# Kernel tuning notes

Hardware: AMD Instinct MI355X
Metric: run time of the kernel (lower is better)

The kernel has to match this reference:

```python
import jax, jax.numpy as jnp
import numpy as np


def setup_inputs() -> dict:
    key = jax.random.key(0)
    ks = jax.random.split(key, 16)
    B, S, D = 2, 2048, 1024
    H, SH, RH = 16, 1, 3
    hd = D // H
    w = 1.0 / np.sqrt(D)
    return {
        "x": jax.random.normal(ks[0], (B, S, D), jnp.float32),
        "Wq": jax.random.normal(ks[1], (D, D), jnp.float32) * w,
        "bq": jnp.zeros((D,), jnp.float32),
        "Wk": jax.random.normal(ks[2], (D, D), jnp.float32) * w,
        "bk": jnp.zeros((D,), jnp.float32),
        "Wv": jax.random.normal(ks[3], (D, D), jnp.float32) * w,
        "bv": jnp.zeros((D,), jnp.float32),
        "Wproj": jax.random.normal(ks[4], (D, D), jnp.float32) * w,
        "bproj": jnp.zeros((D,), jnp.float32),
        "Wr": jax.random.normal(ks[5], (D, H - SH), jnp.float32) * w,
        "br": jnp.zeros((H - SH,), jnp.float32),
        "Ws": jax.random.normal(ks[6], (D, 2), jnp.float32) * w,
        "bs": jnp.zeros((2,), jnp.float32),
        "temperature": jnp.zeros((H, 1, 1), jnp.float32),
        "query_embedding": jax.random.truncated_normal(ks[7], -2.0, 2.0, (H, 1, hd), jnp.float32) * 0.02,
        "num_heads": H,
        "shared_heads": SH,
        "routed_heads": RH,
    }


def reference(x, Wq, bq, Wk, bk, Wv, bv, Wproj, bproj, Wr, br, Ws, bs,
              temperature, query_embedding, num_heads, shared_heads, routed_heads):
    B, S, D = x.shape
    H = num_heads
    hd = D // H

    def split_heads(t):  # [B,S,D] -> [B,H,S,hd]
        return t.reshape(B, S, H, hd).transpose(0, 2, 1, 3)

    q = split_heads(x @ Wq + bq)
    k = split_heads(x @ Wk + bk)
    v = split_heads(x @ Wv + bv)

    # L2-normalize q along head_dim, add learned query embedding, scale by softplus(temperature)
    q_norm = q * jax.lax.rsqrt(jnp.sum(q * q, axis=-1, keepdims=True) + 1e-12)
    q_scaled = (q_norm + query_embedding[None]) * jax.nn.softplus(temperature)[None]

    attn = jnp.einsum('bhqd,bhkd->bhqk', q_scaled, k) / jnp.sqrt(jnp.float32(hd))
    attn = jax.nn.softmax(attn, axis=-1)
    o = jnp.einsum('bhqk,bhkd->bhqd', attn, v)
    o = o.transpose(0, 2, 1, 3).reshape(B, S, D)  # [B,S,D]

    # Routed-head gating via top-k router
    gates = jax.nn.softmax(o @ Wr + br, axis=-1)          # [B,S,H-SH]
    _, idx = jax.lax.top_k(gates, routed_heads)           # [B,S,RH]
    mask = jax.nn.one_hot(idx, H - shared_heads, dtype=gates.dtype).sum(axis=2)
    routed_gates = gates * mask * jnp.float32(routed_heads)

    # Shared-head gating
    sw = jax.nn.softmax(o @ Ws + bs, axis=-1)             # [B,S,2]
    shared_gates = sw * jnp.float32(shared_heads)
    w0 = sw * 2.0
    shared_gates = w0[..., 0:1] * shared_gates
    routed_gates = w0[..., 1:2] * routed_gates
    masked_gates = jnp.concatenate([shared_gates, routed_gates], axis=-1)

    # einsum('bnh,bnd->bnd') sums over h: scales o by sum of gates
    o = masked_gates.sum(axis=-1, keepdims=True) * o
    return o @ Wproj + bproj
```

## Files before the change

kernel.cpp:

```cpp
#include <hip/hip_runtime.h>
#include <hip/hip_bf16.h>

typedef unsigned short ushort_t;
typedef unsigned int uint_t;

typedef __attribute__((ext_vector_type(8))) short bf8;
typedef __attribute__((ext_vector_type(4))) float f4;
typedef __attribute__((ext_vector_type(16))) float f16v;

__device__ __forceinline__ float bf2f(ushort_t u) {
    unsigned int x = ((unsigned int)u) << 16;
    return __uint_as_float(x);
}
__device__ __forceinline__ ushort_t f2bf(float f) {
    unsigned int x = __float_as_uint(f);
    unsigned int r = x + 0x7fffu + ((x >> 16) & 1u);
    return (ushort_t)(r >> 16);
}
__device__ __forceinline__ uint_t pack2bf(float a, float b) {
    return (uint_t)f2bf(a) | ((uint_t)f2bf(b) << 16);
}
__device__ __forceinline__ uint_t pack2bf_fast(float a, float b) {
    uint_t au = __float_as_uint(a) + 0x8000u;
    uint_t bu = __float_as_uint(b) + 0x8000u;
    return __builtin_amdgcn_perm(bu, au, 0x07060302);
}
__device__ __forceinline__ float exp2_fast(float x) {
    float r; asm("v_exp_f32 %0, %1" : "=v"(r) : "v"(x)); return r;
}
__device__ __forceinline__ uint_t cvtpk_bf16(float lo, float hi) {
    uint_t r; asm("v_cvt_pk_bf16_f32 %0, %1, %2" : "=v"(r) : "v"(lo), "v"(hi)); return r;
}
__device__ __forceinline__ void pl32swap(uint_t &a, uint_t &b) {
    asm("v_permlane32_swap_b32 %0, %1" : "+v"(a), "+v"(b));
}

__device__ __forceinline__ void gl2lds16(const ushort_t* g, ushort_t* l) {
    __builtin_amdgcn_global_load_lds(
        (const __attribute__((address_space(1))) void*)g,
        (__attribute__((address_space(3))) void*)l, 16, 0, 0);
}

__global__ __launch_bounds__(256)
void prep(const float* __restrict__ x, ushort_t* __restrict__ xb,
          const float* __restrict__ Wr, const float* __restrict__ Ws,
          ushort_t* __restrict__ Wg,
          const float* __restrict__ W0, const float* __restrict__ W1,
          const float* __restrict__ W2, const float* __restrict__ W3,
          ushort_t* __restrict__ T0, ushort_t* __restrict__ T1,
          ushort_t* __restrict__ T2, ushort_t* __restrict__ T3)
{
    __shared__ float tile[32][33];
    int bid = blockIdx.x;
    int t = threadIdx.x;
    if (bid < 4096) {
        int i = bid * 256 + t;
        float4 v = ((const float4*)x)[i];
        uint2 o;
        o.x = pack2bf(v.x, v.y);
        o.y = pack2bf(v.z, v.w);
        ((uint2*)xb)[i] = o;
    } else if (bid < 4224) {
        int idx = (bid - 4096) * 256 + t;
        int c = idx >> 10, d = idx & 1023;
        float v = 0.f;
        if (c < 15) v = Wr[(size_t)d * 15 + c];
        else if (c < 17) v = Ws[(size_t)d * 2 + (c - 15)];
        Wg[idx] = f2bf(v);
    } else {
        int idx = bid - 4224;
        int z = idx >> 10, r10 = idx & 1023;
        int k0 = (r10 & 31) * 32, n0 = (r10 >> 5) * 32;
        const float* W; ushort_t* T;
        switch (z) {
            case 0: W = W0; T = T0; break;
            case 1: W = W1; T = T1; break;
            case 2: W = W2; T = T2; break;
            default: W = W3; T = T3; break;
        }
        int r = t >> 3, c4 = (t & 7) * 4;
        float4 v = *(const float4*)&W[(size_t)(k0 + r) * 1024 + n0 + c4];
        tile[r][c4 + 0] = v.x; tile[r][c4 + 1] = v.y;
        tile[r][c4 + 2] = v.z; tile[r][c4 + 3] = v.w;
        __syncthreads();
        int n = t >> 3, kk = (t & 7) * 4;
        uint2 o;
        o.x = pack2bf(tile[kk][n], tile[kk + 1][n]);
        o.y = pack2bf(tile[kk + 2][n], tile[kk + 3][n]);
        *(uint2*)&T[(size_t)(n0 + n) * 1024 + k0 + kk] = o;
    }
}

__global__ __launch_bounds__(256)
void gemmQKV(const ushort_t* __restrict__ A, const ushort_t* __restrict__ Wt3,
             const float* __restrict__ bq, const float* __restrict__ bk,
             const float* __restrict__ bv,
             ushort_t* __restrict__ Qb, ushort_t* __restrict__ Kw,
             ushort_t* __restrict__ VTw,
             const float* __restrict__ temp, const float* __restrict__ emb)
{
    const int K = 1024;
    __shared__ ushort_t As[128 * 64];
    __shared__ ushort_t Bs[128 * 64];

    int t = threadIdx.x;
    int m0 = blockIdx.x * 128;
    int y = blockIdx.y;
    int region = y >> 3;
    int n0 = (y & 7) * 128;

    int lane = t & 63, w = t >> 6;
    int lm = lane & 15, quad = lane >> 4;
    int wm = (w >> 1) * 64, wn = (w & 1) * 64;

    f4 acc[4][4] = {};

    int srow = t >> 3;
    int schunk = ((t & 7) ^ (srow & 7)) * 8;
    const ushort_t* pA = &A[(size_t)(m0 + srow) * K + schunk];
    const ushort_t* pB = &Wt3[(size_t)(y * 128 + srow) * K + schunk];
    const size_t rstep = (size_t)32 * K;

    for (int k0 = 0; k0 < K; k0 += 64) {
        #pragma unroll
        for (int j = 0; j < 4; j++) {
            gl2lds16(pA + j * rstep, &As[(t + j * 256) * 8]);
            gl2lds16(pB + j * rstep, &Bs[(t + j * 256) * 8]);
        }
        pA += 64; pB += 64;
        __syncthreads();

        #pragma unroll
        for (int ks = 0; ks < 2; ks++) {
            int rc = ((ks * 4 + quad) ^ (lm & 7)) * 8;
            bf8 af[4], bfr[4];
            #pragma unroll
            for (int mi = 0; mi < 4; mi++)
                af[mi] = *(bf8*)&As[(wm + mi * 16 + lm) * 64 + rc];
            #pragma unroll
            for (int ni = 0; ni < 4; ni++)
                bfr[ni] = *(bf8*)&Bs[(wn + ni * 16 + lm) * 64 + rc];
            if (region == 2) {
                #pragma unroll
                for (int mi = 0; mi < 4; mi++)
                #pragma unroll
                for (int ni = 0; ni < 4; ni++)
                    acc[mi][ni] = __builtin_amdgcn_mfma_f32_16x16x32_bf16(af[mi], bfr[ni], acc[mi][ni], 0, 0, 0);
            } else {
                #pragma unroll
                for (int ni = 0; ni < 4; ni++)
                #pragma unroll
                for (int mi = 0; mi < 4; mi++)
                    acc[ni][mi] = __builtin_amdgcn_mfma_f32_16x16x32_bf16(bfr[ni], af[mi], acc[ni][mi], 0, 0, 0);
            }
        }
        __syncthreads();
    }

    if (region == 0) {
        int head = (n0 + wn) >> 6;
        float sp = log1pf(__expf(temp[head]));
        float qs = sp * 0.18033688011112042f;
        f4 bv4[4], ev4[4];
        #pragma unroll
        for (int ni = 0; ni < 4; ni++) {
            bv4[ni] = *(const f4*)&bq[n0 + wn + ni * 16 + quad * 4];
            ev4[ni] = *(const f4*)&emb[head * 64 + ni * 16 + quad * 4];
        }
        #pragma unroll
        for (int mi = 0; mi < 4; mi++) {
            float v[4][4];
            float ss = 0.f;
            #pragma unroll
            for (int ni = 0; ni < 4; ni++)
            #pragma unroll
            for (int i = 0; i < 4; i++) {
                v[ni][i] = acc[ni][mi][i] + bv4[ni][i];
                ss += v[ni][i] * v[ni][i];
            }
            ss += __shfl_xor(ss, 16, 64);
            ss += __shfl_xor(ss, 32, 64);
            float rs = rsqrtf(ss + 1e-12f);
            int tok = m0 + wm + mi * 16 + lm;
            int b = tok >> 11, s = tok & 2047;
            size_t rowb = (((size_t)(b * 16 + head)) * 2048 + s) * 64;
            #pragma unroll
            for (int ni = 0; ni < 4; ni++) {
                uint2 o;
                o.x = pack2bf((v[ni][0] * rs + ev4[ni][0]) * qs,
                              (v[ni][1] * rs + ev4[ni][1]) * qs);
                o.y = pack2bf((v[ni][2] * rs + ev4[ni][2]) * qs,
                              (v[ni][3] * rs + ev4[ni][3]) * qs);
                *(uint2*)&Qb[rowb + ni * 16 + quad * 4] = o;
            }
        }
    } else if (region == 1) {
        int head = (n0 + wn) >> 6;
        f4 bv4[4];
        #pragma unroll
        for (int ni = 0; ni < 4; ni++)
            bv4[ni] = *(const f4*)&bk[n0 + wn + ni * 16 + quad * 4];
        #pragma unroll
        for (int mi = 0; mi < 4; mi++) {
            int tok = m0 + wm + mi * 16 + lm;
            int b = tok >> 11, s = tok & 2047;
            size_t rowb = (((size_t)(b * 16 + head)) * 2048 + s) * 64;
            #pragma unroll
            for (int ni = 0; ni < 4; ni++) {
                uint2 o;
                o.x = pack2bf(acc[ni][mi][0] + bv4[ni][0], acc[ni][mi][1] + bv4[ni][1]);
                o.y = pack2bf(acc[ni][mi][2] + bv4[ni][2], acc[ni][mi][3] + bv4[ni][3]);
                *(uint2*)&Kw[rowb + ni * 16 + quad * 4] = o;
            }
        }
    } else {
        float bvv[4];
        #pragma unroll
        for (int ni = 0; ni < 4; ni++) bvv[ni] = bv[n0 + wn + ni * 16 + lm];
        #pragma unroll
        for (int mi = 0; mi < 4; mi++) {
            int gr0 = m0 + wm + mi * 16 + quad * 4;
            int b = gr0 >> 11, s0 = gr0 & 2047;
            #pragma unroll
            for (int ni = 0; ni < 4; ni++) {
                int gc = n0 + wn + ni * 16 + lm;
                int h = gc >> 6, d = gc & 63;
                uint2 o;
                o.x = pack2bf(acc[mi][ni][0] + bvv[ni], acc[mi][ni][1] + bvv[ni]);
                o.y = pack2bf(acc[mi][ni][2] + bvv[ni], acc[mi][ni][3] + bvv[ni]);
                *(uint2*)&VTw[(((size_t)(b * 16 + h)) * 64 + d) * 2048 + s0] = o;
            }
        }
    }
}

__global__ __launch_bounds__(256)
void gemmP(const ushort_t* __restrict__ A, const ushort_t* __restrict__ Wt,
           const float* __restrict__ bias, const float* __restrict__ G,
           float* __restrict__ out, int M, int N, int K)
{
    __shared__ ushort_t As[128 * 64];
    __shared__ ushort_t Bs[128 * 64];

    int t = threadIdx.x;
    int m0 = blockIdx.x * 128, n0 = blockIdx.y * 128;
    int lane = t & 63, w = t >> 6;
    int lm = lane & 15, quad = lane >> 4;
    int wm = (w >> 1) * 64, wn = (w & 1) * 64;

    f4 acc[4][4] = {};

    int srow = t >> 3;
    int schunk = ((t & 7) ^ (srow & 7)) * 8;
    const ushort_t* pA = &A[(size_t)(m0 + srow) * K + schunk];
    const ushort_t* pB = &Wt[(size_t)(n0 + srow) * K + schunk];
    const size_t rstep = (size_t)32 * K;

    for (int k0 = 0; k0 < K; k0 += 64) {
        #pragma unroll
        for (int j = 0; j < 4; j++) {
            gl2lds16(pA + j * rstep, &As[(t + j * 256) * 8]);
            gl2lds16(pB + j * rstep, &Bs[(t + j * 256) * 8]);
        }
        pA += 64; pB += 64;
        __syncthreads();

        #pragma unroll
        for (int ks = 0; ks < 2; ks++) {
            int rc = ((ks * 4 + quad) ^ (lm & 7)) * 8;
            bf8 af[4], bfr[4];
            #pragma unroll
            for (int mi = 0; mi < 4; mi++)
                af[mi] = *(bf8*)&As[(wm + mi * 16 + lm) * 64 + rc];
            #pragma unroll
            for (int ni = 0; ni < 4; ni++)
                bfr[ni] = *(bf8*)&Bs[(wn + ni * 16 + lm) * 64 + rc];
            #pragma unroll
            for (int ni = 0; ni < 4; ni++)
            #pragma unroll
            for (int mi = 0; mi < 4; mi++)
                acc[ni][mi] = __builtin_amdgcn_mfma_f32_16x16x32_bf16(bfr[ni], af[mi], acc[ni][mi], 0, 0, 0);
        }
        __syncthreads();
    }

    f4 bv4[4];
    #pragma unroll
    for (int ni = 0; ni < 4; ni++)
        bv4[ni] = *(const f4*)&bias[n0 + wn + ni * 16 + quad * 4];
    #pragma unroll
    for (int mi = 0; mi < 4; mi++) {
        int tok = m0 + wm + mi * 16 + lm;
        float g = G[tok];
        size_t rowb = (size_t)tok * N + n0 + wn;
        #pragma unroll
        for (int ni = 0; ni < 4; ni++) {
            f4 o;
            #pragma unroll
            for (int i = 0; i < 4; i++) o[i] = g * acc[ni][mi][i] + bv4[ni][i];
            *(f4*)&out[rowb + ni * 16 + quad * 4] = o;
        }
    }
}

__global__ __launch_bounds__(256)
void attn(const ushort_t* __restrict__ Q, const ushort_t* __restrict__ K,
          const ushort_t* __restrict__ VT, ushort_t* __restrict__ Opart,
          float* __restrict__ Lw)
{
    __shared__ ushort_t Ks[64 * 72];
    __shared__ ushort_t Vt[64 * 72];

    int t = threadIdx.x, lane = t & 63, w = t >> 6;
    int l31 = lane & 31;
    uint_t hi = lane >> 5;
    int bid = blockIdx.x;
    int bh = bid & 31, qt = (bid >> 5) & 15, ks = bid >> 9;
    size_t base = (size_t)bh * 2048 * 64;

    int tok = qt * 128 + w * 32 + l31;
    const ushort_t* qp = &Q[base + (size_t)tok * 64 + hi * 8];
    bf8 qa[4];
    #pragma unroll
    for (int c = 0; c < 4; c++) qa[c] = *(const bf8*)(qp + c * 16);

    float l_part = 0.f;
    f16v o_acc[2] = {};

    int sr = t >> 3, sc = (t & 7) * 8;
    const ushort_t* kp = &K[base + (size_t)(ks * 1024 + sr) * 64 + sc];
    const ushort_t* vp = &VT[base + (size_t)sr * 2048 + ks * 1024 + sc];

    uint4 rk0 = *(const uint4*)(kp);
    uint4 rk1 = *(const uint4*)(kp + 32 * 64);
    uint4 rv0 = *(const uint4*)(vp);
    uint4 rv1 = *(const uint4*)(vp + 32 * 2048);
    kp += 64 * 64; vp += 64;

    for (int it = 0; it < 16; ++it) {
        *(uint4*)&Ks[sr * 72 + sc] = rk0;
        *(uint4*)&Ks[(sr + 32) * 72 + sc] = rk1;
        *(uint4*)&Vt[sr * 72 + sc] = rv0;
        *(uint4*)&Vt[(sr + 32) * 72 + sc] = rv1;
        __syncthreads();

        rk0 = *(const uint4*)(kp);
        rk1 = *(const uint4*)(kp + 32 * 64);
        rv0 = *(const uint4*)(vp);
        rv1 = *(const uint4*)(vp + 32 * 2048);
        kp += 64 * 64; vp += 64;

        bf8 pf[4];
        #pragma unroll
        for (int kt2 = 0; kt2 < 2; kt2++) {
            f16v s = {};
            #pragma unroll
            for (int c = 0; c < 4; c++) {
                bf8 kf = *(bf8*)&Ks[(kt2 * 32 + l31) * 72 + c * 16 + hi * 8];
                s = __builtin_amdgcn_mfma_f32_32x32x16_bf16(kf, qa[c], s, 0, 0, 0);
            }
            uint_t px[4], py[4];
            #pragma unroll
            for (int g = 0; g < 4; g++) {
                float p0 = exp2_fast(s[g * 4 + 0]);
                float p1 = exp2_fast(s[g * 4 + 1]);
                float p2 = exp2_fast(s[g * 4 + 2]);
                float p3 = exp2_fast(s[g * 4 + 3]);
                l_part += (p0 + p1) + (p2 + p3);
                px[g] = cvtpk_bf16(p0, p1);
                py[g] = cvtpk_bf16(p2, p3);
            }
            #pragma unroll
            for (int cc = 0; cc < 2; cc++) {
                uint_t ax = px[2 * cc], bx = px[2 * cc + 1];
                uint_t ay = py[2 * cc], by = py[2 * cc + 1];
                pl32swap(ax, bx);
                pl32swap(ay, by);
                uint4 u;
                u.x = ax; u.y = ay; u.z = bx; u.w = by;
                pf[kt2 * 2 + cc] = *(bf8*)&u;
            }
        }

        #pragma unroll
        for (int c = 0; c < 4; c++) {
            #pragma unroll
            for (int dt = 0; dt < 2; dt++) {
                bf8 vf = *(bf8*)&Vt[(dt * 32 + l31) * 72 + c * 16 + hi * 8];
                o_acc[dt] = __builtin_amdgcn_mfma_f32_32x32x16_bf16(vf, pf[c], o_acc[dt], 0, 0, 0);
            }
        }
        __syncthreads();
    }

    l_part += __shfl_xor(l_part, 32, 64);
    if (hi == 0) Lw[((size_t)ks * 32 + bh) * 2048 + tok] = l_part;

    size_t pbase = (((size_t)(ks * 32 + bh)) * 2048 + tok) * 64;
    #pragma unroll
    for (int dt = 0; dt < 2; dt++)
    #pragma unroll
    for (int g = 0; g < 4; g++) {
        int d0 = dt * 32 + g * 8 + hi * 4;
        uint2 o;
        o.x = pack2bf_fast(o_acc[dt][g * 4 + 0], o_acc[dt][g * 4 + 1]);
        o.y = pack2bf_fast(o_acc[dt][g * 4 + 2], o_acc[dt][g * 4 + 3]);
        *(uint2*)&Opart[pbase + d0] = o;
    }
}

__global__ __launch_bounds__(256)
void combine(const ushort_t* __restrict__ Opart, const float* __restrict__ Lw,
             ushort_t* __restrict__ Ob)
{
    int i = blockIdx.x * 256 + threadIdx.x;
    int flat = i * 4;
    int row = flat >> 6;
    int d = flat & 63;
    int bh = row >> 11, tok = row & 2047;
    int b = bh >> 4, h = bh & 15;
    float rl = 1.f / (Lw[row] + Lw[65536 + row]);
    uint2 p0 = *(const uint2*)&Opart[flat];
    uint2 p1 = *(const uint2*)&Opart[4194304 + flat];
    float v0 = (bf2f(p0.x & 0xffff) + bf2f(p1.x & 0xffff)) * rl;
    float v1 = (bf2f(p0.x >> 16)   + bf2f(p1.x >> 16))   * rl;
    float v2 = (bf2f(p0.y & 0xffff) + bf2f(p1.y & 0xffff)) * rl;
    float v3 = (bf2f(p0.y >> 16)   + bf2f(p1.y >> 16))   * rl;
    uint2 o;
    o.x = pack2bf(v0, v1);
    o.y = pack2bf(v2, v3);
    *(uint2*)&Ob[((size_t)(b * 2048 + tok)) * 1024 + h * 64 + d] = o;
}

__global__ __launch_bounds__(256)
void router(const ushort_t* __restrict__ O, const ushort_t* __restrict__ Wg,
            const float* __restrict__ br, const float* __restrict__ bs,
            float* __restrict__ G)
{
    __shared__ float Ls[64][21];
    int t = threadIdx.x, lane = t & 63, w = t >> 6;
    int lm = lane & 15, quad = lane >> 4;
    int tok0 = blockIdx.x * 64;

    const ushort_t* ap = &O[(size_t)(tok0 + w * 16 + lm) * 1024 + quad * 8];
    const ushort_t* b0p = &Wg[(size_t)lm * 1024 + quad * 8];
    const ushort_t* b1p = &Wg[(size_t)(16 + lm) * 1024 + quad * 8];

    f4 acc0 = {}, acc1 = {};
    for (int k0 = 0; k0 < 1024; k0 += 32) {
        bf8 a = *(const bf8*)(ap + k0);
        bf8 b0 = *(const bf8*)(b0p + k0);
        bf8 b1 = *(const bf8*)(b1p + k0);
        acc0 = __builtin_amdgcn_mfma_f32_16x16x32_bf16(a, b0, acc0, 0, 0, 0);
        acc1 = __builtin_amdgcn_mfma_f32_16x16x32_bf16(a, b1, acc1, 0, 0, 0);
    }
    #pragma unroll
    for (int i = 0; i < 4; i++) {
        int tl = w * 16 + quad * 4 + i;
        Ls[tl][lm] = acc0[i];
        if (lm == 0) Ls[tl][16] = acc1[i];
    }
    __syncthreads();
    if (t < 64) {
        float v[15];
        float mx = -1e30f;
        #pragma unroll
        for (int c = 0; c < 15; c++) { v[c] = Ls[t][c] + br[c]; mx = fmaxf(mx, v[c]); }
        float sum = 0.f;
        #pragma unroll
        for (int c = 0; c < 15; c++) { v[c] = __expf(v[c] - mx); sum += v[c]; }
        float inv = 1.f / sum;
        float t3 = 0.f;
        for (int r = 0; r < 3; r++) {
            int bi = 0; float bv = -1e30f;
            #pragma unroll
            for (int c = 0; c < 15; c++) if (v[c] > bv) { bv = v[c]; bi = c; }
            t3 += bv; v[bi] = -1e30f;
        }
        t3 *= inv;
        float a0 = Ls[t][15] + bs[0], a1 = Ls[t][16] + bs[1];
        float m2 = fmaxf(a0, a1);
        float e0 = __expf(a0 - m2), e1 = __expf(a1 - m2);
        G[tok0 + t] = (2.f * e0 + 6.f * e1 * t3) / (e0 + e1);
    }
}

extern "C" void kernel_launch(void* const* d_in, const int* in_sizes, int n_in,
                              void* d_out, int out_size, void* d_ws, size_t ws_size,
                              hipStream_t stream)
{
    const float* x     = (const float*)d_in[0];
    const float* Wq    = (const float*)d_in[1];
    const float* bq    = (const float*)d_in[2];
    const float* Wk    = (const float*)d_in[3];
    const float* bk    = (const float*)d_in[4];
    const float* Wv    = (const float*)d_in[5];
    const float* bv    = (const float*)d_in[6];
    const float* Wproj = (const float*)d_in[7];
    const float* bproj = (const float*)d_in[8];
    const float* Wr    = (const float*)d_in[9];
    const float* br    = (const float*)d_in[10];
    const float* Ws    = (const float*)d_in[11];
    const float* bs    = (const float*)d_in[12];
    const float* temp  = (const float*)d_in[13];
    const float* emb   = (const float*)d_in[14];

    const int M = 4096, N = 1024, Kd = 1024;

    char* ws = (char*)d_ws;
    ushort_t* Kw    = (ushort_t*)ws;
    ushort_t* VTw   = (ushort_t*)(ws + 8388608);
    ushort_t* Qb    = (ushort_t*)(ws + 16777216);
    ushort_t* Wtp   = (ushort_t*)(ws + 25165824);
    float*    Gw    = (float*)(ws + 27262976);
    ushort_t* Wg    = (ushort_t*)(ws + 27279360);
    float*    Lw    = (float*)(ws + 27344896);
    ushort_t* Wt3   = (ushort_t*)(ws + 27869184);
    ushort_t* xb    = (ushort_t*)(ws + 34160640);
    ushort_t* Opart = (ushort_t*)(ws + 27869184);
    ushort_t* Ob    = Qb;

    prep<<<8320, 256, 0, stream>>>(x, xb, Wr, Ws, Wg, Wq, Wk, Wv, Wproj,
        Wt3, Wt3 + 1048576, Wt3 + 2097152, Wtp);

    gemmQKV<<<dim3(32, 24), 256, 0, stream>>>(xb, Wt3, bq, bk, bv,
        Qb, Kw, VTw, temp, emb);

    attn<<<1024, 256, 0, stream>>>(Qb, Kw, VTw, Opart, Lw);

    combine<<<4096, 256, 0, stream>>>(Opart, Lw, Ob);

    router<<<64, 256, 0, stream>>>(Ob, Wg, br, bs, Gw);

    gemmP<<<dim3(32, 8), 256, 0, stream>>>(Ob, Wtp, bproj, Gw, (float*)d_out, M, N, Kd);
}
```

Measured before the change: 245.2 us.

## Double-buffer LDS tiles with async prefetch in QKV and projection GEMMs

Both GEMM kernels move from single-buffered LDS tiles, which loaded and synchronized every K step, to two LDS buffers. Each iteration loads all fragments for the tile into registers, issues the global-to-LDS loads for tile kt+2 into the freed buffer, then runs the MFMAs at raised priority. Explicit vmcnt/lgkmcnt waits and barriers replace __syncthreads, so global loads overlap with compute. LDS use doubles to 64KB per block, which may reduce occupancy, and fragment registers double.

```diff
diff --git a/kernel.cpp b/kernel.cpp
--- a/kernel.cpp
+++ b/kernel.cpp
@@ -39,6 +39,19 @@
     __builtin_amdgcn_global_load_lds(
         (const __attribute__((address_space(1))) void*)g,
         (__attribute__((address_space(3))) void*)l, 16, 0, 0);
+}
+
+__device__ __forceinline__ void waitv8() {
+    asm volatile("s_waitcnt vmcnt(8)" ::: "memory");
+    __builtin_amdgcn_sched_barrier(0);
+}
+__device__ __forceinline__ void waitv0() {
+    asm volatile("s_waitcnt vmcnt(0)" ::: "memory");
+    __builtin_amdgcn_sched_barrier(0);
+}
+__device__ __forceinline__ void waitl0() {
+    asm volatile("s_waitcnt lgkmcnt(0)" ::: "memory");
+    __builtin_amdgcn_sched_barrier(0);
 }
 
 __global__ __launch_bounds__(256)
@@ -100,8 +113,9 @@
              const float* __restrict__ temp, const float* __restrict__ emb)
 {
     const int K = 1024;
-    __shared__ ushort_t As[128 * 64];
-    __shared__ ushort_t Bs[128 * 64];
+    const int NT = 16;
+    __shared__ ushort_t As[2][128 * 64];
+    __shared__ ushort_t Bs[2][128 * 64];
 
     int t = threadIdx.x;
     int m0 = blockIdx.x * 128;
@@ -117,44 +131,76 @@
 
     int srow = t >> 3;
     int schunk = ((t & 7) ^ (srow & 7)) * 8;
-    const ushort_t* pA = &A[(size_t)(m0 + srow) * K + schunk];
-    const ushort_t* pB = &Wt3[(size_t)(y * 128 + srow) * K + schunk];
+    const ushort_t* pA0 = &A[(size_t)(m0 + srow) * K + schunk];
+    const ushort_t* pB0 = &Wt3[(size_t)(y * 128 + srow) * K + schunk];
     const size_t rstep = (size_t)32 * K;
 
-    for (int k0 = 0; k0 < K; k0 += 64) {
-        #pragma unroll
-        for (int j = 0; j < 4; j++) {
-            gl2lds16(pA + j * rstep, &As[(t + j * 256) * 8]);
-            gl2lds16(pB + j * rstep, &Bs[(t + j * 256) * 8]);
-        }
-        pA += 64; pB += 64;
-        __syncthreads();
-
+    #pragma unroll
+    for (int j = 0; j < 4; j++) {
+        gl2lds16(pA0 + j * rstep, &As[0][(t + j * 256) * 8]);
+        gl2lds16(pB0 + j * rstep, &Bs[0][(t + j * 256) * 8]);
+    }
+    __builtin_amdgcn_sched_barrier(0);
+    #pragma unroll
+    for (int j = 0; j < 4; j++) {
+        gl2lds16(pA0 + 64 + j * rstep, &As[1][(t + j * 256) * 8]);
+        gl2lds16(pB0 + 64 + j * rstep, &Bs[1][(t + j * 256) * 8]);
+    }
+    __builtin_amdgcn_sched_barrier(0);
+    waitv8();
+    __builtin_amdgcn_s_barrier();
+
+    int cur = 0;
+    for (int kt = 0; kt < NT; ++kt) {
+        bf8 af[2][4], bfr[2][4];
         #pragma unroll
         for (int ks = 0; ks < 2; ks++) {
             int rc = ((ks * 4 + quad) ^ (lm & 7)) * 8;
-            bf8 af[4], bfr[4];
             #pragma unroll
             for (int mi = 0; mi < 4; mi++)
-                af[mi] = *(bf8*)&As[(wm + mi * 16 + lm) * 64 + rc];
+                af[ks][mi] = *(bf8*)&As[cur][(wm + mi * 16 + lm) * 64 + rc];
             #pragma unroll
             for (int ni = 0; ni < 4; ni++)
-                bfr[ni] = *(bf8*)&Bs[(wn + ni * 16 + lm) * 64 + rc];
+                bfr[ks][ni] = *(bf8*)&Bs[cur][(wn + ni * 16 + lm) * 64 + rc];
+        }
+        waitl0();
+        __builtin_amdgcn_s_barrier();
+
+        if (kt + 2 < NT) {
+            const ushort_t* sA = pA0 + (kt + 2) * 64;
+            const ushort_t* sB = pB0 + (kt + 2) * 64;
+            #pragma unroll
+            for (int j = 0; j < 4; j++) {
+                gl2lds16(sA + j * rstep, &As[cur][(t + j * 256) * 8]);
+                gl2lds16(sB + j * rstep, &Bs[cur][(t + j * 256) * 8]);
+            }
+        }
+        __builtin_amdgcn_sched_barrier(0);
+
+        __builtin_amdgcn_s_setprio(1);
+        #pragma unroll
+        for (int ks = 0; ks < 2; ks++) {
             if (region == 2) {
                 #pragma unroll
                 for (int mi = 0; mi < 4; mi++)
                 #pragma unroll
                 for (int ni = 0; ni < 4; ni++)
-                    acc[mi][ni] = __builtin_amdgcn_mfma_f32_16x16x32_bf16(af[mi], bfr[ni], acc[mi][ni], 0, 0, 0);
+                    acc[mi][ni] = __builtin_amdgcn_mfma_f32_16x16x32_bf16(af[ks][mi], bfr[ks][ni], acc[mi][ni], 0, 0, 0);
             } else {
                 #pragma unroll
                 for (int ni = 0; ni < 4; ni++)
                 #pragma unroll
                 for (int mi = 0; mi < 4; mi++)
-                    acc[ni][mi] = __builtin_amdgcn_mfma_f32_16x16x32_bf16(bfr[ni], af[mi], acc[ni][mi], 0, 0, 0);
-            }
-        }
-        __syncthreads();
+                    acc[ni][mi] = __builtin_amdgcn_mfma_f32_16x16x32_bf16(bfr[ks][ni], af[ks][mi], acc[ni][mi], 0, 0, 0);
+            }
+        }
+        __builtin_amdgcn_s_setprio(0);
+        __builtin_amdgcn_sched_barrier(0);
+
+        if (kt + 2 < NT) waitv8();
+        else             waitv0();
+        __builtin_amdgcn_s_barrier();
+        cur ^= 1;
     }
 
     if (region == 0) {
@@ -239,8 +285,9 @@
            const float* __restrict__ bias, const float* __restrict__ G,
            float* __restrict__ out, int M, int N, int K)
 {
-    __shared__ ushort_t As[128 * 64];
-    __shared__ ushort_t Bs[128 * 64];
+    const int NT = 16;
+    __shared__ ushort_t As[2][128 * 64];
+    __shared__ ushort_t Bs[2][128 * 64];
 
     int t = threadIdx.x;
     int m0 = blockIdx.x * 128, n0 = blockIdx.y * 128;
@@ -252,36 +299,68 @@
 
     int srow = t >> 3;
     int schunk = ((t & 7) ^ (srow & 7)) * 8;
-    const ushort_t* pA = &A[(size_t)(m0 + srow) * K + schunk];
-    const ushort_t* pB = &Wt[(size_t)(n0 + srow) * K + schunk];
+    const ushort_t* pA0 = &A[(size_t)(m0 + srow) * K + schunk];
+    const ushort_t* pB0 = &Wt[(size_t)(n0 + srow) * K + schunk];
     const size_t rstep = (size_t)32 * K;
 
-    for (int k0 = 0; k0 < K; k0 += 64) {
-        #pragma unroll
-        for (int j = 0; j < 4; j++) {
-            gl2lds16(pA + j * rstep, &As[(t + j * 256) * 8]);
-            gl2lds16(pB + j * rstep, &Bs[(t + j * 256) * 8]);
-        }
-        pA += 64; pB += 64;
-        __syncthreads();
-
+    #pragma unroll
+    for (int j = 0; j < 4; j++) {
+        gl2lds16(pA0 + j * rstep, &As[0][(t + j * 256) * 8]);
+        gl2lds16(pB0 + j * rstep, &Bs[0][(t + j * 256) * 8]);
+    }
+    __builtin_amdgcn_sched_barrier(0);
+    #pragma unroll
+    for (int j = 0; j < 4; j++) {
+        gl2lds16(pA0 + 64 + j * rstep, &As[1][(t + j * 256) * 8]);
+        gl2lds16(pB0 + 64 + j * rstep, &Bs[1][(t + j * 256) * 8]);
+    }
+    __builtin_amdgcn_sched_barrier(0);
+    waitv8();
+    __builtin_amdgcn_s_barrier();
+
+    int cur = 0;
+    for (int kt = 0; kt < NT; ++kt) {
+        bf8 af[2][4], bfr[2][4];
         #pragma unroll
         for (int ks = 0; ks < 2; ks++) {
             int rc = ((ks * 4 + quad) ^ (lm & 7)) * 8;
-            bf8 af[4], bfr[4];
             #pragma unroll
             for (int mi = 0; mi < 4; mi++)
-                af[mi] = *(bf8*)&As[(wm + mi * 16 + lm) * 64 + rc];
+                af[ks][mi] = *(bf8*)&As[cur][(wm + mi * 16 + lm) * 64 + rc];
             #pragma unroll
             for (int ni = 0; ni < 4; ni++)
-                bfr[ni] = *(bf8*)&Bs[(wn + ni * 16 + lm) * 64 + rc];
+                bfr[ks][ni] = *(bf8*)&Bs[cur][(wn + ni * 16 + lm) * 64 + rc];
+        }
+        waitl0();
+        __builtin_amdgcn_s_barrier();
+
+        if (kt + 2 < NT) {
+            const ushort_t* sA = pA0 + (kt + 2) * 64;
+            const ushort_t* sB = pB0 + (kt + 2) * 64;
+            #pragma unroll
+            for (int j = 0; j < 4; j++) {
+                gl2lds16(sA + j * rstep, &As[cur][(t + j * 256) * 8]);
+                gl2lds16(sB + j * rstep, &Bs[cur][(t + j * 256) * 8]);
+            }
+        }
+        __builtin_amdgcn_sched_barrier(0);
+
+        __builtin_amdgcn_s_setprio(1);
+        #pragma unroll
+        for (int ks = 0; ks < 2; ks++) {
             #pragma unroll
             for (int ni = 0; ni < 4; ni++)
             #pragma unroll
             for (int mi = 0; mi < 4; mi++)
-                acc[ni][mi] = __builtin_amdgcn_mfma_f32_16x16x32_bf16(bfr[ni], af[mi], acc[ni][mi], 0, 0, 0);
-        }
-        __syncthreads();
+                acc[ni][mi] = __builtin_amdgcn_mfma_f32_16x16x32_bf16(bfr[ks][ni], af[ks][mi], acc[ni][mi], 0, 0, 0);
+        }
+        __builtin_amdgcn_s_setprio(0);
+        __builtin_amdgcn_sched_barrier(0);
+
+        if (kt + 2 < NT) waitv8();
+        else             waitv0();
+        __builtin_amdgcn_s_barrier();
+        cur ^= 1;
     }
 
     f4 bv4[4];
```

New measurement: 248.3 us. About the same (+1.3%).

## Fuse split-K combine with router and remap GEMM blocks for XCD locality

Applied to the files above, without the earlier changes.

Merges the combine and router kernels into one kernel. Each block merges the split-K attention partials for 16 tokens, keeps the bf16 rows in LDS, and runs the router MFMA and gating softmax/top-k from there, so Ob is not re-read from global memory. It also flattens the GEMM grids and remaps block indices so that blocks on the same XCD (index mod 8) work on nearby M/N tiles, aiming for better L2 reuse. The trade-off is that the fused kernel launches only 256 blocks and one wave does the serial router GEMM while the other three wait, so it may run below full occupancy.

```diff
diff --git a/kernel.cpp b/kernel.cpp
--- a/kernel.cpp
+++ b/kernel.cpp
@@ -39,6 +39,11 @@
     __builtin_amdgcn_global_load_lds(
         (const __attribute__((address_space(1))) void*)g,
         (__attribute__((address_space(3))) void*)l, 16, 0, 0);
+}
+
+__device__ __forceinline__ void waitl0() {
+    asm volatile("s_waitcnt lgkmcnt(0)" ::: "memory");
+    __builtin_amdgcn_sched_barrier(0);
 }
 
 __global__ __launch_bounds__(256)
@@ -104,8 +109,13 @@
     __shared__ ushort_t Bs[128 * 64];
 
     int t = threadIdx.x;
-    int m0 = blockIdx.x * 128;
-    int y = blockIdx.y;
+    int n = blockIdx.x;
+    int c = n & 7, m = n >> 3;
+    int cx = c & 3, cy = c >> 2;
+    int xi = m & 7, yi = m >> 3;
+    int bx = cx * 8 + xi;
+    int y  = cy * 12 + yi;
+    int m0 = bx * 128;
     int region = y >> 3;
     int n0 = (y & 7) * 128;
 
@@ -243,7 +253,12 @@
     __shared__ ushort_t Bs[128 * 64];
 
     int t = threadIdx.x;
-    int m0 = blockIdx.x * 128, n0 = blockIdx.y * 128;
+    int nIdx = blockIdx.x;
+    int c = nIdx & 7, m = nIdx >> 3;
+    int xi = m & 3, yi = m >> 2;
+    int m0 = (c * 4 + xi) * 128;
+    int n0 = yi * 128;
+
     int lane = t & 63, w = t >> 6;
     int lm = lane & 15, quad = lane >> 4;
     int wm = (w >> 1) * 64, wn = (w & 1) * 64;
@@ -410,78 +425,89 @@
 }
 
 __global__ __launch_bounds__(256)
-void combine(const ushort_t* __restrict__ Opart, const float* __restrict__ Lw,
-             ushort_t* __restrict__ Ob)
-{
-    int i = blockIdx.x * 256 + threadIdx.x;
-    int flat = i * 4;
-    int row = flat >> 6;
-    int d = flat & 63;
-    int bh = row >> 11, tok = row & 2047;
-    int b = bh >> 4, h = bh & 15;
-    float rl = 1.f / (Lw[row] + Lw[65536 + row]);
-    uint2 p0 = *(const uint2*)&Opart[flat];
-    uint2 p1 = *(const uint2*)&Opart[4194304 + flat];
-    float v0 = (bf2f(p0.x & 0xffff) + bf2f(p1.x & 0xffff)) * rl;
-    float v1 = (bf2f(p0.x >> 16)   + bf2f(p1.x >> 16))   * rl;
-    float v2 = (bf2f(p0.y & 0xffff) + bf2f(p1.y & 0xffff)) * rl;
-    float v3 = (bf2f(p0.y >> 16)   + bf2f(p1.y >> 16))   * rl;
-    uint2 o;
-    o.x = pack2bf(v0, v1);
-    o.y = pack2bf(v2, v3);
-    *(uint2*)&Ob[((size_t)(b * 2048 + tok)) * 1024 + h * 64 + d] = o;
-}
-
-__global__ __launch_bounds__(256)
-void router(const ushort_t* __restrict__ O, const ushort_t* __restrict__ Wg,
-            const float* __restrict__ br, const float* __restrict__ bs,
+void fuseCR(const ushort_t* __restrict__ Opart, const float* __restrict__ Lw,
+            const ushort_t* __restrict__ Wg, const float* __restrict__ br,
+            const float* __restrict__ bs, ushort_t* __restrict__ Ob,
             float* __restrict__ G)
 {
-    __shared__ float Ls[64][21];
-    int t = threadIdx.x, lane = t & 63, w = t >> 6;
-    int lm = lane & 15, quad = lane >> 4;
-    int tok0 = blockIdx.x * 64;
-
-    const ushort_t* ap = &O[(size_t)(tok0 + w * 16 + lm) * 1024 + quad * 8];
-    const ushort_t* b0p = &Wg[(size_t)lm * 1024 + quad * 8];
-    const ushort_t* b1p = &Wg[(size_t)(16 + lm) * 1024 + quad * 8];
-
-    f4 acc0 = {}, acc1 = {};
-    for (int k0 = 0; k0 < 1024; k0 += 32) {
-        bf8 a = *(const bf8*)(ap + k0);
-        bf8 b0 = *(const bf8*)(b0p + k0);
-        bf8 b1 = *(const bf8*)(b1p + k0);
-        acc0 = __builtin_amdgcn_mfma_f32_16x16x32_bf16(a, b0, acc0, 0, 0, 0);
-        acc1 = __builtin_amdgcn_mfma_f32_16x16x32_bf16(a, b1, acc1, 0, 0, 0);
-    }
-    #pragma unroll
-    for (int i = 0; i < 4; i++) {
-        int tl = w * 16 + quad * 4 + i;
-        Ls[tl][lm] = acc0[i];
-        if (lm == 0) Ls[tl][16] = acc1[i];
+    __shared__ ushort_t Obs[16 * 1032];
+    __shared__ float rl_s[16][16];
+    __shared__ float Ls[16][21];
+
+    int t = threadIdx.x;
+    int tokg0 = blockIdx.x * 16;
+    int b = tokg0 >> 11, st0 = tokg0 & 2047;
+
+    {
+        int h = t >> 4, tt = t & 15;
+        size_t row = (size_t)(b * 16 + h) * 2048 + st0 + tt;
+        rl_s[h][tt] = 1.f / (Lw[row] + Lw[65536 + row]);
     }
     __syncthreads();
+
+    {
+        int tt = t >> 4, dc = (t & 15) * 4;
+        #pragma unroll 4
+        for (int h = 0; h < 16; h++) {
+            size_t rbase = ((size_t)(b * 16 + h) * 2048 + st0 + tt) * 64 + dc;
+            uint2 p0 = *(const uint2*)&Opart[rbase];
+            uint2 p1 = *(const uint2*)&Opart[4194304 + rbase];
+            float rl = rl_s[h][tt];
+            float v0 = (bf2f(p0.x & 0xffff) + bf2f(p1.x & 0xffff)) * rl;
+            float v1 = (bf2f(p0.x >> 16)   + bf2f(p1.x >> 16))   * rl;
+            float v2 = (bf2f(p0.y & 0xffff) + bf2f(p1.y & 0xffff)) * rl;
+            float v3 = (bf2f(p0.y >> 16)   + bf2f(p1.y >> 16))   * rl;
+            uint2 o;
+            o.x = pack2bf(v0, v1);
+            o.y = pack2bf(v2, v3);
+            *(uint2*)&Obs[tt * 1032 + h * 64 + dc] = o;
+            *(uint2*)&Ob[((size_t)(tokg0 + tt)) * 1024 + h * 64 + dc] = o;
+        }
+    }
+    __syncthreads();
+
     if (t < 64) {
-        float v[15];
-        float mx = -1e30f;
-        #pragma unroll
-        for (int c = 0; c < 15; c++) { v[c] = Ls[t][c] + br[c]; mx = fmaxf(mx, v[c]); }
-        float sum = 0.f;
-        #pragma unroll
-        for (int c = 0; c < 15; c++) { v[c] = __expf(v[c] - mx); sum += v[c]; }
-        float inv = 1.f / sum;
-        float t3 = 0.f;
-        for (int r = 0; r < 3; r++) {
-            int bi = 0; float bv = -1e30f;
-            #pragma unroll
-            for (int c = 0; c < 15; c++) if (v[c] > bv) { bv = v[c]; bi = c; }
-            t3 += bv; v[bi] = -1e30f;
-        }
-        t3 *= inv;
-        float a0 = Ls[t][15] + bs[0], a1 = Ls[t][16] + bs[1];
-        float m2 = fmaxf(a0, a1);
-        float e0 = __expf(a0 - m2), e1 = __expf(a1 - m2);
-        G[tok0 + t] = (2.f * e0 + 6.f * e1 * t3) / (e0 + e1);
+        int lm = t & 15, quad = t >> 4;
+        const ushort_t* b0p = &Wg[(size_t)lm * 1024 + quad * 8];
+        const ushort_t* b1p = &Wg[(size_t)(16 + lm) * 1024 + quad * 8];
+        f4 acc0 = {}, acc1 = {};
+        for (int k0 = 0; k0 < 1024; k0 += 32) {
+            bf8 a  = *(const bf8*)&Obs[lm * 1032 + k0 + quad * 8];
+            bf8 b0 = *(const bf8*)(b0p + k0);
+            bf8 b1 = *(const bf8*)(b1p + k0);
+            acc0 = __builtin_amdgcn_mfma_f32_16x16x32_bf16(a, b0, acc0, 0, 0, 0);
+            acc1 = __builtin_amdgcn_mfma_f32_16x16x32_bf16(a, b1, acc1, 0, 0, 0);
+        }
+        #pragma unroll
+        for (int i = 0; i < 4; i++) {
+            int tl = quad * 4 + i;
+            Ls[tl][lm] = acc0[i];
+            if (lm == 0) Ls[tl][16] = acc1[i];
+        }
+        waitl0();
+
+        if (t < 16) {
+            float v[15];
+            float mx = -1e30f;
+            #pragma unroll
+            for (int c = 0; c < 15; c++) { v[c] = Ls[t][c] + br[c]; mx = fmaxf(mx, v[c]); }
+            float sum = 0.f;
+            #pragma unroll
+            for (int c = 0; c < 15; c++) { v[c] = __expf(v[c] - mx); sum += v[c]; }
+            float inv = 1.f / sum;
+            float t3 = 0.f;
+            for (int r = 0; r < 3; r++) {
+                int bi = 0; float bv = -1e30f;
+                #pragma unroll
+                for (int c = 0; c < 15; c++) if (v[c] > bv) { bv = v[c]; bi = c; }
+                t3 += bv; v[bi] = -1e30f;
+            }
+            t3 *= inv;
+            float a0 = Ls[t][15] + bs[0], a1 = Ls[t][16] + bs[1];
+            float m2 = fmaxf(a0, a1);
+            float e0 = __expf(a0 - m2), e1 = __expf(a1 - m2);
+            G[tokg0 + t] = (2.f * e0 + 6.f * e1 * t3) / (e0 + e1);
+        }
     }
 }
 
@@ -523,14 +549,12 @@
     prep<<<8320, 256, 0, stream>>>(x, xb, Wr, Ws, Wg, Wq, Wk, Wv, Wproj,
         Wt3, Wt3 + 1048576, Wt3 + 2097152, Wtp);
 
-    gemmQKV<<<dim3(32, 24), 256, 0, stream>>>(xb, Wt3, bq, bk, bv,
+    gemmQKV<<<768, 256, 0, stream>>>(xb, Wt3, bq, bk, bv,
         Qb, Kw, VTw, temp, emb);
 
     attn<<<1024, 256, 0, stream>>>(Qb, Kw, VTw, Opart, Lw);
 
-    combine<<<4096, 256, 0, stream>>>(Opart, Lw, Ob);
-
-    router<<<64, 256, 0, stream>>>(Ob, Wg, br, bs, Gw);
-
-    gemmP<<<dim3(32, 8), 256, 0, stream>>>(Ob, Wtp, bproj, Gw, (float*)d_out, M, N, Kd);
-}
+    fuseCR<<<256, 256, 0, stream>>>(Opart, Lw, Wg, br, bs, Ob, Gw);
+
+    gemmP<<<256, 256, 0, stream>>>(Ob, Wtp, bproj, Gw, (float*)d_out, M, N, Kd);
+}
```

After: 262.7 us. 7.1% more time.
